# Kernel tuning notes

Hardware: AMD Instinct MI355X
Metric: run time of the kernel (lower is better)

Reference implementation:

```python
import jax, jax.numpy as jnp
import numpy as np

N, E = 50000, 800000
IN, HID, OUT, L = 512, 64, 40, 16
ALPHA, LAMBDA = 0.1, 0.5


def setup_inputs() -> dict:
    key = jax.random.key(0)
    ks = jax.random.split(key, 8)
    features = jax.random.normal(ks[0], (N, IN), jnp.float32)
    src = jax.random.randint(ks[1], (E,), 0, N)
    dst = jax.random.randint(ks[2], (E,), 0, N)
    # fcs[0]: Linear(IN, HID); fcs[1]: Linear(HID, OUT)
    W_in = jax.random.normal(ks[3], (IN, HID), jnp.float32) / np.sqrt(IN)
    b_in = jnp.zeros((HID,), jnp.float32)
    W_out = jax.random.normal(ks[4], (HID, OUT), jnp.float32) / np.sqrt(HID)
    b_out = jnp.zeros((OUT,), jnp.float32)
    # per-layer GCN2Conv weights (project_initial_features=False -> weight1 & weight2) + bias
    W1 = jax.random.normal(ks[5], (L, HID, HID), jnp.float32) / np.sqrt(HID)
    W2 = jax.random.normal(ks[6], (L, HID, HID), jnp.float32) / np.sqrt(HID)
    b = jnp.zeros((L, HID), jnp.float32)
    return dict(features=features, W_in=W_in, b_in=b_in, W1=W1, W2=W2, b=b,
                W_out=W_out, b_out=b_out, src=src, dst=dst)


def reference(features, W_in, b_in, W1, W2, b, W_out, b_out, src, dst):
    ones = jnp.ones((E,), jnp.float32)
    deg_out = jax.ops.segment_sum(ones, src, num_segments=N)
    deg_in = jax.ops.segment_sum(ones, dst, num_segments=N)
    norm_src = jnp.maximum(deg_out, 1.0) ** -0.5  # [N]
    norm_dst = jnp.maximum(deg_in, 1.0) ** -0.5   # [N]
    betas = jnp.log(LAMBDA / jnp.arange(1, L + 1, dtype=jnp.float32) + 1.0)

    # inference: dropout is identity
    h0 = jax.nn.relu(features @ W_in + b_in)  # [N, HID]

    def layer(h, params):
        w1, w2, bias, beta = params
        # symmetric-normalized sparse propagation: D^-1/2 A D^-1/2 h
        hs = h * norm_src[:, None]
        agg = jax.ops.segment_sum(hs[src], dst, num_segments=N) * norm_dst[:, None]
        f = (1.0 - ALPHA) * agg   # smoothed part
        f0 = ALPHA * h0           # initial residual
        rst = (1.0 - beta) * f + beta * (f @ w1)
        rst = rst + (1.0 - beta) * f0 + beta * (f0 @ w2)
        rst = rst + bias
        return jax.nn.relu(rst), None

    h, _ = jax.lax.scan(layer, h0, (W1, W2, b, betas))
    logits = h @ W_out + b_out  # [N, OUT]
    return jax.nn.log_softmax(logits, axis=1)
```

## Files before the change

kernel.cpp:

```cpp
#include <hip/hip_runtime.h>
#include <math.h>

#define NN 50000
#define NE 800000
#define INF 512
#define HID 64
#define OUTF 40
#define NL 16

#define NBLK 256
#define EPB 3125
#define NBUK 196
#define SLEN (NBUK * NBLK)

#define TN 32
#define FP 72

using short8 = __attribute__((ext_vector_type(8))) short;
using f32x4v = __attribute__((ext_vector_type(4))) float;

__device__ __forceinline__ unsigned int f2bf(float f) {
    unsigned int u = __float_as_uint(f);
    return (u + 0x7fffu + ((u >> 16) & 1u)) >> 16;
}
__device__ __forceinline__ float bflo(unsigned int w) { return __uint_as_float(w << 16); }
__device__ __forceinline__ float bfhi(unsigned int w) { return __uint_as_float(w & 0xffff0000u); }
__device__ __forceinline__ float bfs(unsigned short u) { return __uint_as_float(((unsigned)u) << 16); }


__global__ __launch_bounds__(256) void k_cnt(const int* __restrict__ src, const int* __restrict__ dst,
                                             int* __restrict__ cntD, int* __restrict__ cntS) {
    __shared__ int hD[NBUK];
    __shared__ int hS[NBUK];
    int t = threadIdx.x;
    int blk = blockIdx.x;
    if (t < NBUK) { hD[t] = 0; hS[t] = 0; }
    __syncthreads();
    int s0 = blk * EPB;
    for (int i = t; i < EPB; i += 256) {
        int e = s0 + i;
        atomicAdd(&hD[dst[e] >> 8], 1);
        atomicAdd(&hS[src[e] >> 8], 1);
    }
    __syncthreads();
    if (t < NBUK) {
        cntD[t * NBLK + blk] = hD[t];
        cntS[t * NBLK + blk] = hS[t];
    }
}

__global__ __launch_bounds__(256) void gscanA(const int* __restrict__ in, int* __restrict__ incl,
                                              int* __restrict__ bsum, int len) {
    __shared__ int lds[256];
    int i = blockIdx.x * 256 + threadIdx.x;
    int v = (i < len) ? in[i] : 0;
    lds[threadIdx.x] = v;
    __syncthreads();
    for (int off = 1; off < 256; off <<= 1) {
        int t = (threadIdx.x >= off) ? lds[threadIdx.x - off] : 0;
        __syncthreads();
        lds[threadIdx.x] += t;
        __syncthreads();
    }
    if (i < len) incl[i] = lds[threadIdx.x];
    if (threadIdx.x == 255) bsum[blockIdx.x] = lds[255];
}

__global__ __launch_bounds__(256) void gscanB(int* __restrict__ bsum, int nb) {
    __shared__ int lds[256];
    int v = (threadIdx.x < nb) ? bsum[threadIdx.x] : 0;
    lds[threadIdx.x] = v;
    __syncthreads();
    for (int off = 1; off < 256; off <<= 1) {
        int t = (threadIdx.x >= off) ? lds[threadIdx.x - off] : 0;
        __syncthreads();
        lds[threadIdx.x] += t;
        __syncthreads();
    }
    if (threadIdx.x < nb) bsum[threadIdx.x] = lds[threadIdx.x] - v;
}

__global__ __launch_bounds__(256) void gscanC(const int* __restrict__ incl, const int* __restrict__ in,
                                              const int* __restrict__ bsum, int* __restrict__ off, int len) {
    int i = blockIdx.x * 256 + threadIdx.x;
    if (i < len) off[i] = incl[i] - in[i] + bsum[i >> 8];
}

__global__ __launch_bounds__(256) void k_scat(const int* __restrict__ src, const int* __restrict__ dst,
                                              const int* __restrict__ offD, const int* __restrict__ offS,
                                              uint2* __restrict__ edst, int* __restrict__ esrc) {
    __shared__ int cD[NBUK];
    __shared__ int cS[NBUK];
    int t = threadIdx.x;
    int blk = blockIdx.x;
    if (t < NBUK) { cD[t] = 0; cS[t] = 0; }
    __syncthreads();
    int s0 = blk * EPB;
    for (int i = t; i < EPB; i += 256) {
        int e = s0 + i;
        int d = dst[e];
        int s = src[e];
        int bD = d >> 8;
        int r = atomicAdd(&cD[bD], 1);
        uint2 v;
        v.x = (unsigned)d;
        v.y = (unsigned)s;
        edst[offD[bD * NBLK + blk] + r] = v;
        int bS = s >> 8;
        int r2 = atomicAdd(&cS[bS], 1);
        esrc[offS[bS * NBLK + blk] + r2] = s;
    }
}

__global__ __launch_bounds__(256) void k_bcsr(const uint2* __restrict__ edst, const int* __restrict__ offD,
                                              float* __restrict__ nd, int* __restrict__ row_start,
                                              int* __restrict__ col) {
    __shared__ int cnt[256];
    __shared__ int ex[256];
    __shared__ int cur[256];
    int b = blockIdx.x;
    int t = threadIdx.x;
    int base = offD[b * NBLK];
    int end = (b < NBUK - 1) ? offD[(b + 1) * NBLK] : NE;
    cnt[t] = 0;
    __syncthreads();
    for (int p = base + t; p < end; p += 256) {
        uint2 ed = edst[p];
        atomicAdd(&cnt[ed.x & 255], 1);
    }
    __syncthreads();
    int v = cnt[t];
    ex[t] = v;
    __syncthreads();
    for (int off = 1; off < 256; off <<= 1) {
        int tv = (t >= off) ? ex[t - off] : 0;
        __syncthreads();
        ex[t] += tv;
        __syncthreads();
    }
    int excl = ex[t] - v;
    cur[t] = excl;
    int node = b * 256 + t;
    if (node < NN) {
        nd[node] = 1.0f / sqrtf((float)max(v, 1));
        row_start[node] = base + excl;
    }
    __syncthreads();
    for (int p = base + t; p < end; p += 256) {
        uint2 ed = edst[p];
        int r = atomicAdd(&cur[ed.x & 255], 1);
        col[base + r] = (int)ed.y;
    }
}

__global__ __launch_bounds__(256) void k_bns(const int* __restrict__ esrc, const int* __restrict__ offS,
                                             float* __restrict__ ns) {
    __shared__ int cnt[256];
    int b = blockIdx.x;
    int t = threadIdx.x;
    int base = offS[b * NBLK];
    int end = (b < NBUK - 1) ? offS[(b + 1) * NBLK] : NE;
    cnt[t] = 0;
    __syncthreads();
    for (int p = base + t; p < end; p += 256) {
        atomicAdd(&cnt[esrc[p] & 255], 1);
    }
    __syncthreads();
    int node = b * 256 + t;
    if (node < NN) ns[node] = 1.0f / sqrtf((float)max(cnt[t], 1));
}


__global__ __launch_bounds__(256) void k_wcat(const float* __restrict__ W1, const float* __restrict__ W2,
                                              unsigned short* __restrict__ wc) {
    int o = blockIdx.x * 256 + threadIdx.x;
    if (o >= NL * 4 * 4 * 64 * 8) return;
    int j = o & 7;
    int ln = (o >> 3) & 63;
    int c = (o >> 9) & 3;
    int s = (o >> 11) & 3;
    int l = o >> 13;
    int colg = c * 16 + (ln & 15);
    int k = (s & 1) * 32 + ((ln >> 4) << 3) + j;
    float beta = logf(0.5f / (float)(l + 1) + 1.0f);
    const float* W = (s < 2) ? W1 : W2;
    wc[o] = (unsigned short)f2bf(beta * W[((size_t)l * 64 + k) * 64 + colg]);
}

__global__ __launch_bounds__(256) void k_wfrag(const float* __restrict__ Win, unsigned short* __restrict__ wf) {
    int o = blockIdx.x * 256 + threadIdx.x;
    if (o < 16 * 4 * 64 * 8) {
        int jj = o & 7;
        int l = (o >> 3) & 63;
        int c = (o >> 9) & 3;
        int s = o >> 11;
        int colg = c * 16 + (l & 15);
        int k = s * 32 + ((l >> 4) << 3) + jj;
        wf[o] = (unsigned short)f2bf(Win[k * HID + colg]);
    }
}

__global__ __launch_bounds__(256) void k_gemm0(const float* __restrict__ feat, const unsigned short* __restrict__ wf,
                                               float* __restrict__ p0, float* __restrict__ p1) {
    __shared__ unsigned int fS[2048];
    int tid = threadIdx.x;
    int lane = tid & 63;
    int wv = tid >> 6;
    int bx = blockIdx.x;
    int w = bx >> 1;
    int kh = bx & 1;
    int nb = w * 64;
    f32x4v acc[4];
#pragma unroll
    for (int c = 0; c < 4; c++) acc[c] = {0.0f, 0.0f, 0.0f, 0.0f};

    int k0 = kh * 256;
    for (int kc = k0; kc < k0 + 256; kc += 64) {
        if (kc != k0) __syncthreads();
        float4 t[4];
#pragma unroll
        for (int j = 0; j < 4; j++) {
            int i = tid + j * 256;
            int nl = i >> 4;
            int k4 = i & 15;
            int n = min(nb + nl, NN - 1);
            t[j] = *(const float4*)(feat + (size_t)n * INF + kc + k4 * 4);
        }
#pragma unroll
        for (int j = 0; j < 4; j++) {
            int i = tid + j * 256;
            int nl = i >> 4;
            int kl = (i & 15) * 4;
            int s = kl >> 5;
            int kk = kl & 31;
            int lslot = (nl & 15) | ((kk >> 3) << 4);
            int dstu = (((s * 4 + (nl >> 4)) * 64 + lslot) << 2) + ((kk & 4) >> 1);
            fS[dstu] = f2bf(t[j].x) | (f2bf(t[j].y) << 16);
            fS[dstu + 1] = f2bf(t[j].z) | (f2bf(t[j].w) << 16);
        }
        __syncthreads();
#pragma unroll
        for (int s = 0; s < 2; ++s) {
            int sg = (kc + s * 32) >> 5;
            short8 af = *(const short8*)&fS[((s * 4 + wv) * 64 + lane) << 2];
            short8 bf[4];
#pragma unroll
            for (int c = 0; c < 4; ++c)
                bf[c] = *(const short8*)(wf + ((size_t)(sg * 4 + c) * 64 + lane) * 8);
#pragma unroll
            for (int c = 0; c < 4; ++c)
                acc[c] = __builtin_amdgcn_mfma_f32_16x16x32_bf16(af, bf[c], acc[c], 0, 0, 0);
        }
    }
    float* p = kh ? p1 : p0;
    int nodeb = nb + (wv << 4) + ((lane >> 4) << 2);
    int colb = lane & 15;
#pragma unroll
    for (int r = 0; r < 4; ++r) {
        int node = nodeb + r;
        if (node < NN) {
            float* pp = p + (size_t)node * HID + colb;
#pragma unroll
            for (int c = 0; c < 4; ++c) pp[c * 16] = acc[c][r];
        }
    }
}

__global__ __launch_bounds__(256) void k_gfin(const float* __restrict__ p0, const float* __restrict__ p1,
                                              const float* __restrict__ bin, const float* __restrict__ ns,
                                              unsigned int* __restrict__ hs, unsigned int* __restrict__ f0b) {
    int i = blockIdx.x * 256 + threadIdx.x;
    if (i >= NN * 16) return;
    int node = i >> 4;
    int q = i & 15;
    float4 a = ((const float4*)p0)[i];
    float4 b = ((const float4*)p1)[i];
    float4 bi = ((const float4*)bin)[q];
    float nsv = ns[node];
    float q0 = fmaxf(a.x + b.x + bi.x, 0.0f);
    float q1 = fmaxf(a.y + b.y + bi.y, 0.0f);
    float q2 = fmaxf(a.z + b.z + bi.z, 0.0f);
    float q3 = fmaxf(a.w + b.w + bi.w, 0.0f);
    uint2 pk;
    pk.x = f2bf(q0 * nsv) | (f2bf(q1 * nsv) << 16);
    pk.y = f2bf(q2 * nsv) | (f2bf(q3 * nsv) << 16);
    *(uint2*)(hs + (size_t)node * 32 + q * 2) = pk;
    uint2 pf;
    pf.x = f2bf(q0 * 0.1f) | (f2bf(q1 * 0.1f) << 16);
    pf.y = f2bf(q2 * 0.1f) | (f2bf(q3 * 0.1f) << 16);
    *(uint2*)(f0b + (size_t)node * 32 + q * 2) = pf;
}

__global__ __launch_bounds__(256) void k_layer(const unsigned int* __restrict__ hs_in, const int* __restrict__ col,
                                               const int* __restrict__ row_start,
                                               const float* __restrict__ nd, const unsigned int* __restrict__ f0b,
                                               const unsigned short* __restrict__ wc, const float* __restrict__ bias,
                                               const float* __restrict__ ns, float omb,
                                               float* __restrict__ h, unsigned int* __restrict__ hs_out, int write_h) {
    __shared__ unsigned short fS[TN * FP];
    __shared__ unsigned short f0S[TN * FP];
    __shared__ unsigned short oS[TN * FP];
    __shared__ float nsS[TN];
    int tid = threadIdx.x;
    int lane = tid & 63;
    int wv = tid >> 6;
    int nb = blockIdx.x * TN;
    int g = lane >> 4;
    int ql = lane & 15;

    {
        int nl = tid >> 3, sg = tid & 7;
        int n = min(nb + nl, NN - 1);
        uint4 v = *(const uint4*)(f0b + (size_t)n * 32 + sg * 4);
        *(uint4*)&f0S[nl * FP + sg * 8] = v;
    }
    if (tid < TN) nsS[tid] = ns[min(nb + tid, NN - 1)];

    int nlP[2], baseP[2], degP[2], idxP[2];
    float ndP[2];
#pragma unroll
    for (int p = 0; p < 2; ++p) {
        int nl = p * 16 + wv * 4 + g;
        int n = min(nb + nl, NN - 1);
        nlP[p] = nl;
        int base = row_start[n];
        int nxt = (n < NN - 1) ? row_start[n + 1] : NE;
        baseP[p] = base;
        degP[p] = nxt - base;
        ndP[p] = nd[n];
    }
#pragma unroll
    for (int p = 0; p < 2; ++p) {
        idxP[p] = (ql < min(16, degP[p])) ? col[baseP[p] + ql] : 0;
    }

#pragma unroll
    for (int pass = 0; pass < 2; ++pass) {
        int base = baseP[pass];
        int deg = degP[pass];
        int idxv = idxP[pass];
        float ax = 0.0f, ay = 0.0f, az = 0.0f, aw = 0.0f;
        for (int done = 0; done < deg; done += 16) {
            int cnt = min(16, deg - done);
            int nxt = done + 16;
            int idxn = 0;
            if (nxt < deg && ql < deg - nxt) idxn = col[base + nxt + ql];
            uint2 pv[8];
#pragma unroll
            for (int e = 0; e < 8; ++e) {
                int s = __shfl(idxv, (g << 4) | e, 64);
                uint2 v = {0u, 0u};
                if (e < cnt) v = *(const uint2*)(hs_in + (size_t)s * 32 + ql * 2);
                pv[e] = v;
            }
#pragma unroll
            for (int e = 0; e < 8; ++e) {
                ax += bflo(pv[e].x);
                ay += bfhi(pv[e].x);
                az += bflo(pv[e].y);
                aw += bfhi(pv[e].y);
            }
#pragma unroll
            for (int e = 0; e < 8; ++e) {
                int s = __shfl(idxv, (g << 4) | (8 + e), 64);
                uint2 v = {0u, 0u};
                if (8 + e < cnt) v = *(const uint2*)(hs_in + (size_t)s * 32 + ql * 2);
                pv[e] = v;
            }
#pragma unroll
            for (int e = 0; e < 8; ++e) {
                ax += bflo(pv[e].x);
                ay += bfhi(pv[e].x);
                az += bflo(pv[e].y);
                aw += bfhi(pv[e].y);
            }
            idxv = idxn;
        }
        float sc = 0.9f * ndP[pass];
        int nl = nlP[pass];
        uint2 w;
        w.x = f2bf(ax * sc) | (f2bf(ay * sc) << 16);
        w.y = f2bf(az * sc) | (f2bf(aw * sc) << 16);
        *(uint2*)&fS[nl * FP + ql * 4] = w;
    }
    __syncthreads();

    int hi = lane >> 4;
    int lo = lane & 15;
    f32x4v acc0 = {0.0f, 0.0f, 0.0f, 0.0f};
    f32x4v acc1 = {0.0f, 0.0f, 0.0f, 0.0f};
#pragma unroll
    for (int s = 0; s < 4; ++s) {
        short8 bf = *(const short8*)(wc + ((size_t)(s * 4 + wv) * 64 + lane) * 8);
        const unsigned short* ab = (s < 2) ? fS : f0S;
        int ko = (s & 1) * 32;
        short8 a0 = *(const short8*)&ab[(0 * 16 + lo) * FP + ko + hi * 8];
        short8 a1 = *(const short8*)&ab[(1 * 16 + lo) * FP + ko + hi * 8];
        acc0 = __builtin_amdgcn_mfma_f32_16x16x32_bf16(a0, bf, acc0, 0, 0, 0);
        acc1 = __builtin_amdgcn_mfma_f32_16x16x32_bf16(a1, bf, acc1, 0, 0, 0);
    }

    int colg = wv * 16 + lo;
    float bv = bias[colg];
#pragma unroll
    for (int m = 0; m < 2; ++m) {
        f32x4v a = m ? acc1 : acc0;
#pragma unroll
        for (int r = 0; r < 4; ++r) {
            int rowl = m * 16 + hi * 4 + r;
            float fv = bfs(fS[rowl * FP + colg]);
            float f0v = bfs(f0S[rowl * FP + colg]);
            float q = fmaxf(a[r] + omb * (fv + f0v) + bv, 0.0f);
            oS[rowl * FP + colg] = (unsigned short)f2bf(q * nsS[rowl]);
            if (write_h) {
                int node = nb + rowl;
                if (node < NN) h[(size_t)node * HID + colg] = q;
            }
        }
    }
    __syncthreads();

    {
        int nl = tid >> 3, sg = tid & 7;
        int node = nb + nl;
        if (node < NN) {
            uint4 v = *(const uint4*)&oS[nl * FP + sg * 8];
            *(uint4*)(hs_out + (size_t)node * 32 + sg * 4) = v;
        }
    }
}

__global__ __launch_bounds__(256) void k_out(const float* __restrict__ h, const float* __restrict__ Wout,
                                             const float* __restrict__ bout, float* __restrict__ out) {
    __shared__ float red_mx[4][64];
    __shared__ float red_s[4][64];
    int tid = threadIdx.x;
    int lane = tid & 63;
    int wv = tid >> 6;
    int half = wv & 1;
    int grp = wv >> 1;
    int node = blockIdx.x * 128 + grp * 64 + lane;
    int nodec = min(node, NN - 1);
    float acc[20];
#pragma unroll
    for (int c = 0; c < 20; c++) acc[c] = 0.0f;
    const float4* hr = (const float4*)(h + (size_t)nodec * HID);
    const float* wb = Wout + half * 20;
    for (int kk = 0; kk < HID / 4; ++kk) {
        float4 a = hr[kk];
        float av[4] = {a.x, a.y, a.z, a.w};
#pragma unroll
        for (int j = 0; j < 4; j++) {
            const float* wr = wb + (size_t)(kk * 4 + j) * OUTF;
#pragma unroll
            for (int c = 0; c < 20; c++) acc[c] += av[j] * wr[c];
        }
    }
    const float* bp = bout + half * 20;
#pragma unroll
    for (int c = 0; c < 20; c++) acc[c] += bp[c];
    float mx = acc[0];
#pragma unroll
    for (int c = 1; c < 20; c++) mx = fmaxf(mx, acc[c]);
    red_mx[wv][lane] = mx;
    __syncthreads();
    float gmx = fmaxf(mx, red_mx[wv ^ 1][lane]);
    float s = 0.0f;
#pragma unroll
    for (int c = 0; c < 20; c++) s += expf(acc[c] - gmx);
    red_s[wv][lane] = s;
    __syncthreads();
    float lse = logf(s + red_s[wv ^ 1][lane]) + gmx;
    if (node < NN) {
        float4* op = (float4*)(out + (size_t)node * OUTF + half * 20);
#pragma unroll
        for (int q = 0; q < 5; q++) {
            float4 v;
            v.x = acc[q * 4 + 0] - lse;
            v.y = acc[q * 4 + 1] - lse;
            v.z = acc[q * 4 + 2] - lse;
            v.w = acc[q * 4 + 3] - lse;
            op[q] = v;
        }
    }
}

extern "C" void kernel_launch(void* const* d_in, const int* in_sizes, int n_in,
                              void* d_out, int out_size, void* d_ws, size_t ws_size,
                              hipStream_t stream) {
    const float* feat = (const float*)d_in[0];
    const float* Win  = (const float*)d_in[1];
    const float* bin  = (const float*)d_in[2];
    const float* W1   = (const float*)d_in[3];
    const float* W2   = (const float*)d_in[4];
    const float* bvec = (const float*)d_in[5];
    const float* Wout = (const float*)d_in[6];
    const float* bout = (const float*)d_in[7];
    const int*   src  = (const int*)d_in[8];
    const int*   dst  = (const int*)d_in[9];
    float* out = (float*)d_out;

    char* ws = (char*)d_ws;
    size_t off = 0;
    auto take = [&](size_t bytes) {
        void* p = ws + off;
        off += (bytes + 255) & ~(size_t)255;
        return p;
    };
    int* bsum      = (int*)take(256 * 4);
    int* row_start = (int*)take(NN * 4);
    int* col       = (int*)take(NE * 4);
    float* nsrc    = (float*)take(NN * 4);
    float* ndst    = (float*)take(NN * 4);
    int* cntD      = (int*)take(SLEN * 4);
    int* cntS      = (int*)take(SLEN * 4);
    int* offD      = (int*)take(SLEN * 4);
    int* offS      = (int*)take(SLEN * 4);
    int* sincl     = (int*)take(SLEN * 4);
    unsigned short* wcat  = (unsigned short*)take((size_t)NL * 4 * 4 * 64 * 8 * 2);
    unsigned short* wfrag = (unsigned short*)take((size_t)INF * HID * 2);
    unsigned int* f0b = (unsigned int*)take((size_t)NN * HID * 2);
    float* hbuf    = (float*)take((size_t)NN * HID * 4);
    float* part1   = (float*)take((size_t)NN * HID * 4);
    unsigned int* hsA = (unsigned int*)take((size_t)NN * HID * 2);
    unsigned int* hsB = (unsigned int*)take((size_t)NN * HID * 2);

    uint2* edst = (uint2*)hbuf;
    int* esrc   = (int*)part1;

    const int NB_W = (NN + 63) / 64;
    const int NB_L = (NN + TN - 1) / TN;
    const int NB_O = (NN + 127) / 128;
    const int NB_S = SLEN / 256;

    k_cnt<<<NBLK, 256, 0, stream>>>(src, dst, cntD, cntS);
    gscanA<<<NB_S, 256, 0, stream>>>(cntD, sincl, bsum, SLEN);
    gscanB<<<1, 256, 0, stream>>>(bsum, NB_S);
    gscanC<<<NB_S, 256, 0, stream>>>(sincl, cntD, bsum, offD, SLEN);
    gscanA<<<NB_S, 256, 0, stream>>>(cntS, sincl, bsum, SLEN);
    gscanB<<<1, 256, 0, stream>>>(bsum, NB_S);
    gscanC<<<NB_S, 256, 0, stream>>>(sincl, cntS, bsum, offS, SLEN);
    k_scat<<<NBLK, 256, 0, stream>>>(src, dst, offD, offS, edst, esrc);
    k_bcsr<<<NBUK, 256, 0, stream>>>(edst, offD, ndst, row_start, col);
    k_bns<<<NBUK, 256, 0, stream>>>(esrc, offS, nsrc);

    k_wcat<<<(NL * 4 * 4 * 64 * 8 + 255) / 256, 256, 0, stream>>>(W1, W2, wcat);
    k_wfrag<<<(INF * HID + 255) / 256, 256, 0, stream>>>(Win, wfrag);
    k_gemm0<<<2 * NB_W, 256, 0, stream>>>(feat, wfrag, hbuf, part1);
    k_gfin<<<(NN * 16 + 255) / 256, 256, 0, stream>>>(hbuf, part1, bin, nsrc, hsA, f0b);

    for (int l = 0; l < NL; ++l) {
        const unsigned int* hin = (l & 1) ? hsB : hsA;
        unsigned int* hout = (l & 1) ? hsA : hsB;
        float beta = logf(0.5f / (float)(l + 1) + 1.0f);
        float omb = 1.0f - beta;
        k_layer<<<NB_L, 256, 0, stream>>>(hin, col, row_start, ndst, f0b,
                                          wcat + (size_t)l * 4 * 4 * 64 * 8, bvec + l * HID,
                                          nsrc, omb, hbuf, hout, (l == NL - 1) ? 1 : 0);
    }
    k_out<<<NB_O, 256, 0, stream>>>(hbuf, Wout, bout, out);
}
```

Baseline: 578.9 us.

## Merge preprocessing kernels and widen neighbor gathers to 16-byte loads

The two prefix scans over destination and source bucket counts become one scan over a concatenated array, with an offset correction for the second half. The CSR build and source-degree kernels are merged into one launch, as are the two weight-packing kernels, which cuts the launch count. In the per-layer aggregation, each lane now loads 16 bytes per neighbor, and two half-groups handle alternating edges whose partial sums are combined with an xor shuffle. This is meant to improve memory-level parallelism in the gather, at the cost of extra shuffles and twice as many accumulator registers.

```diff
diff --git a/kernel.cpp b/kernel.cpp
--- a/kernel.cpp
+++ b/kernel.cpp
@@ -29,7 +29,7 @@
 
 
 __global__ __launch_bounds__(256) void k_cnt(const int* __restrict__ src, const int* __restrict__ dst,
-                                             int* __restrict__ cntD, int* __restrict__ cntS) {
+                                             int* __restrict__ cnt2) {
     __shared__ int hD[NBUK];
     __shared__ int hS[NBUK];
     int t = threadIdx.x;
@@ -44,8 +44,8 @@
     }
     __syncthreads();
     if (t < NBUK) {
-        cntD[t * NBLK + blk] = hD[t];
-        cntS[t * NBLK + blk] = hS[t];
+        cnt2[t * NBLK + blk] = hD[t];
+        cnt2[SLEN + t * NBLK + blk] = hS[t];
     }
 }
 
@@ -66,12 +66,12 @@
     if (threadIdx.x == 255) bsum[blockIdx.x] = lds[255];
 }
 
-__global__ __launch_bounds__(256) void gscanB(int* __restrict__ bsum, int nb) {
-    __shared__ int lds[256];
+__global__ __launch_bounds__(512) void gscanB(int* __restrict__ bsum, int nb) {
+    __shared__ int lds[512];
     int v = (threadIdx.x < nb) ? bsum[threadIdx.x] : 0;
     lds[threadIdx.x] = v;
     __syncthreads();
-    for (int off = 1; off < 256; off <<= 1) {
+    for (int off = 1; off < 512; off <<= 1) {
         int t = (threadIdx.x >= off) ? lds[threadIdx.x - off] : 0;
         __syncthreads();
         lds[threadIdx.x] += t;
@@ -83,7 +83,7 @@
 __global__ __launch_bounds__(256) void gscanC(const int* __restrict__ incl, const int* __restrict__ in,
                                               const int* __restrict__ bsum, int* __restrict__ off, int len) {
     int i = blockIdx.x * 256 + threadIdx.x;
-    if (i < len) off[i] = incl[i] - in[i] + bsum[i >> 8];
+    if (i < len) off[i] = incl[i] - in[i] + bsum[i >> 8] - ((i >= SLEN) ? NE : 0);
 }
 
 __global__ __launch_bounds__(256) void k_scat(const int* __restrict__ src, const int* __restrict__ dst,
@@ -112,91 +112,87 @@
     }
 }
 
-__global__ __launch_bounds__(256) void k_bcsr(const uint2* __restrict__ edst, const int* __restrict__ offD,
-                                              float* __restrict__ nd, int* __restrict__ row_start,
-                                              int* __restrict__ col) {
+__global__ __launch_bounds__(256) void k_build(const uint2* __restrict__ edst, const int* __restrict__ esrc,
+                                               const int* __restrict__ offD, const int* __restrict__ offS,
+                                               float* __restrict__ nd, int* __restrict__ row_start,
+                                               int* __restrict__ col, float* __restrict__ ns) {
     __shared__ int cnt[256];
     __shared__ int ex[256];
     __shared__ int cur[256];
-    int b = blockIdx.x;
     int t = threadIdx.x;
-    int base = offD[b * NBLK];
-    int end = (b < NBUK - 1) ? offD[(b + 1) * NBLK] : NE;
-    cnt[t] = 0;
-    __syncthreads();
-    for (int p = base + t; p < end; p += 256) {
-        uint2 ed = edst[p];
-        atomicAdd(&cnt[ed.x & 255], 1);
-    }
-    __syncthreads();
-    int v = cnt[t];
-    ex[t] = v;
-    __syncthreads();
-    for (int off = 1; off < 256; off <<= 1) {
-        int tv = (t >= off) ? ex[t - off] : 0;
-        __syncthreads();
-        ex[t] += tv;
-        __syncthreads();
-    }
-    int excl = ex[t] - v;
-    cur[t] = excl;
-    int node = b * 256 + t;
-    if (node < NN) {
-        nd[node] = 1.0f / sqrtf((float)max(v, 1));
-        row_start[node] = base + excl;
-    }
-    __syncthreads();
-    for (int p = base + t; p < end; p += 256) {
-        uint2 ed = edst[p];
-        int r = atomicAdd(&cur[ed.x & 255], 1);
-        col[base + r] = (int)ed.y;
-    }
-}
-
-__global__ __launch_bounds__(256) void k_bns(const int* __restrict__ esrc, const int* __restrict__ offS,
-                                             float* __restrict__ ns) {
-    __shared__ int cnt[256];
-    int b = blockIdx.x;
-    int t = threadIdx.x;
-    int base = offS[b * NBLK];
-    int end = (b < NBUK - 1) ? offS[(b + 1) * NBLK] : NE;
-    cnt[t] = 0;
-    __syncthreads();
-    for (int p = base + t; p < end; p += 256) {
-        atomicAdd(&cnt[esrc[p] & 255], 1);
-    }
-    __syncthreads();
-    int node = b * 256 + t;
-    if (node < NN) ns[node] = 1.0f / sqrtf((float)max(cnt[t], 1));
-}
-
-
-__global__ __launch_bounds__(256) void k_wcat(const float* __restrict__ W1, const float* __restrict__ W2,
-                                              unsigned short* __restrict__ wc) {
+    if (blockIdx.x < NBUK) {
+        int b = blockIdx.x;
+        int base = offD[b * NBLK];
+        int end = (b < NBUK - 1) ? offD[(b + 1) * NBLK] : NE;
+        cnt[t] = 0;
+        __syncthreads();
+        for (int p = base + t; p < end; p += 256) {
+            uint2 ed = edst[p];
+            atomicAdd(&cnt[ed.x & 255], 1);
+        }
+        __syncthreads();
+        int v = cnt[t];
+        ex[t] = v;
+        __syncthreads();
+        for (int off = 1; off < 256; off <<= 1) {
+            int tv = (t >= off) ? ex[t - off] : 0;
+            __syncthreads();
+            ex[t] += tv;
+            __syncthreads();
+        }
+        int excl = ex[t] - v;
+        cur[t] = excl;
+        int node = b * 256 + t;
+        if (node < NN) {
+            nd[node] = 1.0f / sqrtf((float)max(v, 1));
+            row_start[node] = base + excl;
+        }
+        __syncthreads();
+        for (int p = base + t; p < end; p += 256) {
+            uint2 ed = edst[p];
+            int r = atomicAdd(&cur[ed.x & 255], 1);
+            col[base + r] = (int)ed.y;
+        }
+    } else {
+        int b = blockIdx.x - NBUK;
+        int base = offS[b * NBLK];
+        int end = (b < NBUK - 1) ? offS[(b + 1) * NBLK] : NE;
+        cnt[t] = 0;
+        __syncthreads();
+        for (int p = base + t; p < end; p += 256) {
+            atomicAdd(&cnt[esrc[p] & 255], 1);
+        }
+        __syncthreads();
+        int node = b * 256 + t;
+        if (node < NN) ns[node] = 1.0f / sqrtf((float)max(cnt[t], 1));
+    }
+}
+
+__global__ __launch_bounds__(256) void k_wpp(const float* __restrict__ W1, const float* __restrict__ W2,
+                                             const float* __restrict__ Win,
+                                             unsigned short* __restrict__ wc, unsigned short* __restrict__ wf) {
     int o = blockIdx.x * 256 + threadIdx.x;
-    if (o >= NL * 4 * 4 * 64 * 8) return;
-    int j = o & 7;
-    int ln = (o >> 3) & 63;
-    int c = (o >> 9) & 3;
-    int s = (o >> 11) & 3;
-    int l = o >> 13;
-    int colg = c * 16 + (ln & 15);
-    int k = (s & 1) * 32 + ((ln >> 4) << 3) + j;
-    float beta = logf(0.5f / (float)(l + 1) + 1.0f);
-    const float* W = (s < 2) ? W1 : W2;
-    wc[o] = (unsigned short)f2bf(beta * W[((size_t)l * 64 + k) * 64 + colg]);
-}
-
-__global__ __launch_bounds__(256) void k_wfrag(const float* __restrict__ Win, unsigned short* __restrict__ wf) {
-    int o = blockIdx.x * 256 + threadIdx.x;
-    if (o < 16 * 4 * 64 * 8) {
-        int jj = o & 7;
-        int l = (o >> 3) & 63;
+    const int NWC = NL * 4 * 4 * 64 * 8;
+    if (o < NWC) {
+        int j = o & 7;
+        int ln = (o >> 3) & 63;
         int c = (o >> 9) & 3;
-        int s = o >> 11;
+        int s = (o >> 11) & 3;
+        int l = o >> 13;
+        int colg = c * 16 + (ln & 15);
+        int k = (s & 1) * 32 + ((ln >> 4) << 3) + j;
+        float beta = logf(0.5f / (float)(l + 1) + 1.0f);
+        const float* W = (s < 2) ? W1 : W2;
+        wc[o] = (unsigned short)f2bf(beta * W[((size_t)l * 64 + k) * 64 + colg]);
+    } else if (o < NWC + 16 * 4 * 64 * 8) {
+        int o2 = o - NWC;
+        int jj = o2 & 7;
+        int l = (o2 >> 3) & 63;
+        int c = (o2 >> 9) & 3;
+        int s = o2 >> 11;
         int colg = c * 16 + (l & 15);
         int k = s * 32 + ((l >> 4) << 3) + jj;
-        wf[o] = (unsigned short)f2bf(Win[k * HID + colg]);
+        wf[o2] = (unsigned short)f2bf(Win[k * HID + colg]);
     }
 }
 
@@ -307,6 +303,8 @@
     int nb = blockIdx.x * TN;
     int g = lane >> 4;
     int ql = lane & 15;
+    int half = ql >> 3;
+    int qb = ql & 7;
 
     {
         int nl = tid >> 3, sg = tid & 7;
@@ -339,49 +337,63 @@
         int base = baseP[pass];
         int deg = degP[pass];
         int idxv = idxP[pass];
-        float ax = 0.0f, ay = 0.0f, az = 0.0f, aw = 0.0f;
+        float a0 = 0.f, a1 = 0.f, a2 = 0.f, a3 = 0.f, a4 = 0.f, a5 = 0.f, a6 = 0.f, a7 = 0.f;
         for (int done = 0; done < deg; done += 16) {
             int cnt = min(16, deg - done);
             int nxt = done + 16;
             int idxn = 0;
             if (nxt < deg && ql < deg - nxt) idxn = col[base + nxt + ql];
-            uint2 pv[8];
-#pragma unroll
-            for (int e = 0; e < 8; ++e) {
-                int s = __shfl(idxv, (g << 4) | e, 64);
-                uint2 v = {0u, 0u};
-                if (e < cnt) v = *(const uint2*)(hs_in + (size_t)s * 32 + ql * 2);
+            uint4 pv[4];
+#pragma unroll
+            for (int e = 0; e < 4; ++e) {
+                int ec = 2 * e + half;
+                int s = __shfl(idxv, (g << 4) | ec, 64);
+                uint4 v = {0u, 0u, 0u, 0u};
+                if (ec < cnt) v = *(const uint4*)(hs_in + (size_t)s * 32 + qb * 4);
                 pv[e] = v;
             }
 #pragma unroll
-            for (int e = 0; e < 8; ++e) {
-                ax += bflo(pv[e].x);
-                ay += bfhi(pv[e].x);
-                az += bflo(pv[e].y);
-                aw += bfhi(pv[e].y);
+            for (int e = 0; e < 4; ++e) {
+                a0 += bflo(pv[e].x); a1 += bfhi(pv[e].x);
+                a2 += bflo(pv[e].y); a3 += bfhi(pv[e].y);
+                a4 += bflo(pv[e].z); a5 += bfhi(pv[e].z);
+                a6 += bflo(pv[e].w); a7 += bfhi(pv[e].w);
             }
 #pragma unroll
-            for (int e = 0; e < 8; ++e) {
-                int s = __shfl(idxv, (g << 4) | (8 + e), 64);
-                uint2 v = {0u, 0u};
-                if (8 + e < cnt) v = *(const uint2*)(hs_in + (size_t)s * 32 + ql * 2);
+            for (int e = 0; e < 4; ++e) {
+                int ec = 8 + 2 * e + half;
+                int s = __shfl(idxv, (g << 4) | ec, 64);
+                uint4 v = {0u, 0u, 0u, 0u};
+                if (ec < cnt) v = *(const uint4*)(hs_in + (size_t)s * 32 + qb * 4);
                 pv[e] = v;
             }
 #pragma unroll
-            for (int e = 0; e < 8; ++e) {
-                ax += bflo(pv[e].x);
-                ay += bfhi(pv[e].x);
-                az += bflo(pv[e].y);
-                aw += bfhi(pv[e].y);
+            for (int e = 0; e < 4; ++e) {
+                a0 += bflo(pv[e].x); a1 += bfhi(pv[e].x);
+                a2 += bflo(pv[e].y); a3 += bfhi(pv[e].y);
+                a4 += bflo(pv[e].z); a5 += bfhi(pv[e].z);
+                a6 += bflo(pv[e].w); a7 += bfhi(pv[e].w);
             }
             idxv = idxn;
         }
+        a0 += __shfl_xor(a0, 8, 64);
+        a1 += __shfl_xor(a1, 8, 64);
+        a2 += __shfl_xor(a2, 8, 64);
+        a3 += __shfl_xor(a3, 8, 64);
+        a4 += __shfl_xor(a4, 8, 64);
+        a5 += __shfl_xor(a5, 8, 64);
+        a6 += __shfl_xor(a6, 8, 64);
+        a7 += __shfl_xor(a7, 8, 64);
         float sc = 0.9f * ndP[pass];
         int nl = nlP[pass];
-        uint2 w;
-        w.x = f2bf(ax * sc) | (f2bf(ay * sc) << 16);
-        w.y = f2bf(az * sc) | (f2bf(aw * sc) << 16);
-        *(uint2*)&fS[nl * FP + ql * 4] = w;
+        if (half == 0) {
+            uint4 w;
+            w.x = f2bf(a0 * sc) | (f2bf(a1 * sc) << 16);
+            w.y = f2bf(a2 * sc) | (f2bf(a3 * sc) << 16);
+            w.z = f2bf(a4 * sc) | (f2bf(a5 * sc) << 16);
+            w.w = f2bf(a6 * sc) | (f2bf(a7 * sc) << 16);
+            *(uint4*)&fS[nl * FP + qb * 8] = w;
+        }
     }
     __syncthreads();
 
@@ -507,16 +519,14 @@
         off += (bytes + 255) & ~(size_t)255;
         return p;
     };
-    int* bsum      = (int*)take(256 * 4);
+    int* bsum      = (int*)take(512 * 4);
     int* row_start = (int*)take(NN * 4);
     int* col       = (int*)take(NE * 4);
     float* nsrc    = (float*)take(NN * 4);
     float* ndst    = (float*)take(NN * 4);
-    int* cntD      = (int*)take(SLEN * 4);
-    int* cntS      = (int*)take(SLEN * 4);
-    int* offD      = (int*)take(SLEN * 4);
-    int* offS      = (int*)take(SLEN * 4);
-    int* sincl     = (int*)take(SLEN * 4);
+    int* cnt2      = (int*)take(2 * SLEN * 4);
+    int* off2      = (int*)take(2 * SLEN * 4);
+    int* sincl     = (int*)take(2 * SLEN * 4);
     unsigned short* wcat  = (unsigned short*)take((size_t)NL * 4 * 4 * 64 * 8 * 2);
     unsigned short* wfrag = (unsigned short*)take((size_t)INF * HID * 2);
     unsigned int* f0b = (unsigned int*)take((size_t)NN * HID * 2);
@@ -527,25 +537,22 @@
 
     uint2* edst = (uint2*)hbuf;
     int* esrc   = (int*)part1;
+    int* offD = off2;
+    int* offS = off2 + SLEN;
 
     const int NB_W = (NN + 63) / 64;
     const int NB_L = (NN + TN - 1) / TN;
     const int NB_O = (NN + 127) / 128;
-    const int NB_S = SLEN / 256;
-
-    k_cnt<<<NBLK, 256, 0, stream>>>(src, dst, cntD, cntS);
-    gscanA<<<NB_S, 256, 0, stream>>>(cntD, sincl, bsum, SLEN);
-    gscanB<<<1, 256, 0, stream>>>(bsum, NB_S);
-    gscanC<<<NB_S, 256, 0, stream>>>(sincl, cntD, bsum, offD, SLEN);
-    gscanA<<<NB_S, 256, 0, stream>>>(cntS, sincl, bsum, SLEN);
-    gscanB<<<1, 256, 0, stream>>>(bsum, NB_S);
-    gscanC<<<NB_S, 256, 0, stream>>>(sincl, cntS, bsum, offS, SLEN);
+    const int NB_S2 = 2 * SLEN / 256;
+
+    k_cnt<<<NBLK, 256, 0, stream>>>(src, dst, cnt2);
+    gscanA<<<NB_S2, 256, 0, stream>>>(cnt2, sincl, bsum, 2 * SLEN);
+    gscanB<<<1, 512, 0, stream>>>(bsum, NB_S2);
+    gscanC<<<NB_S2, 256, 0, stream>>>(sincl, cnt2, bsum, off2, 2 * SLEN);
     k_scat<<<NBLK, 256, 0, stream>>>(src, dst, offD, offS, edst, esrc);
-    k_bcsr<<<NBUK, 256, 0, stream>>>(edst, offD, ndst, row_start, col);
-    k_bns<<<NBUK, 256, 0, stream>>>(esrc, offS, nsrc);
-
-    k_wcat<<<(NL * 4 * 4 * 64 * 8 + 255) / 256, 256, 0, stream>>>(W1, W2, wcat);
-    k_wfrag<<<(INF * HID + 255) / 256, 256, 0, stream>>>(Win, wfrag);
+    k_build<<<2 * NBUK, 256, 0, stream>>>(edst, esrc, offD, offS, ndst, row_start, col, nsrc);
+
+    k_wpp<<<(NL * 4 * 4 * 64 * 8 + INF * HID + 255) / 256, 256, 0, stream>>>(W1, W2, Win, wcat, wfrag);
     k_gemm0<<<2 * NB_W, 256, 0, stream>>>(feat, wfrag, hbuf, part1);
     k_gfin<<<(NN * 16 + 255) / 256, 256, 0, stream>>>(hbuf, part1, bin, nsrc, hsA, f0b);
 
```

New measurement: 557.5 us, median of 2. 1.04x faster.
